# Optimization experiments

Hardware: AMD Instinct MI355X
Metric: run time of the kernel (lower is better)

## Reference

```python
import jax, jax.numpy as jnp
import numpy as np

Nc, Nt, K = 32, 64, 2
P = 1.0
BATCH = 4096
EPS_BIS = 1e-5
MAX_ITER = 100


def setup_inputs() -> dict:
    key = jax.random.key(0)
    ks = jax.random.split(key, 5)
    H = jax.random.normal(ks[0], (BATCH, K, Nc, 2 * Nt), dtype=jnp.float32)
    dims = [2 * K * K, 256, 256, 256, 4 * K]
    inp = {"H": H}
    for i in range(4):
        inp[f"W{i}"] = jax.random.normal(ks[1 + i], (dims[i], dims[i + 1]), dtype=jnp.float32) / float(np.sqrt(dims[i]))
        inp[f"b{i}"] = jnp.zeros((dims[i + 1],), dtype=jnp.float32)
    return inp


def _forward(H, W0, b0, W1, b1, W2, b2, W3, b3):
    batch = H.shape[0]
    eyeK = jnp.eye(K, dtype=jnp.complex64)
    # Source quirk: imag slice H[..., :Nt:2*Nt] has step 2*Nt>Nt -> only column 0, broadcast as imag part
    H1 = H[..., :Nt] + 1j * H[..., 0:Nt:2 * Nt]  # [b,K,Nc,Nt] complex64
    # Analog precoder: conj of center-subcarrier channel per user, unit-modulus normalized
    F_RF = jnp.conj(jnp.transpose(H1[:, :, Nc // 2, :], (0, 2, 1)))  # [b,Nt,K]
    F_RF = F_RF / jnp.abs(F_RF) / np.sqrt(Nt)
    # Source quirk: literal reshape (not permute) mixing batch and subcarrier dims
    H1r = H1.reshape(Nc, batch, K, Nt)
    H_equ = jnp.matmul(H1r, F_RF).reshape(batch, Nc, K, K)  # [Nc,b,K,Nt]@[b,Nt,K] -> [Nc,b,K,K]
    power = jnp.sum(jnp.abs(H_equ) ** 2, axis=(2, 3))  # [b,Nc]
    H_equ = H_equ / jnp.sqrt(power)[:, :, None, None]
    Hf = H_equ.reshape(batch, Nc, K * K)
    x = jnp.concatenate([jnp.real(Hf), jnp.imag(Hf)], axis=2)  # [b,Nc,2*K*K]
    # TRANS_BLOCK stand-in: MLP 8->256->256->256->4K
    for (Wl, bl, act) in ((W0, b0, True), (W1, b1, True), (W2, b2, True), (W3, b3, False)):
        x = x @ Wl + bl
        if act:
            x = jax.nn.relu(x)
    U = (x[..., 0:K] + 1j * x[..., K:2 * K]).astype(jnp.complex64)   # [b,Nc,K]
    Wm = (x[..., 2 * K:3 * K] + 1j * x[..., 3 * K:4 * K]).astype(jnp.complex64)
    Hc = H_equ.astype(jnp.complex64)  # H_hat
    coef = Wm * (jnp.abs(U) ** 2)     # [b,Nc,K]
    # B(mu) = sum_k W_k|U_k|^2 conj(h_k) h_k^T + K*mu*I  (mu*I added K times in source loop)
    B_base = jnp.einsum('bnk,bnki,bnkj->bnij', coef, jnp.conj(Hc), Hc)  # [b,Nc,K,K]
    UW = U * Wm

    def compute_V(mu, Bb, uw, hc):
        Bm = Bb + (K * mu) * eyeK
        Binv = jnp.linalg.inv(Bm)  # batched 2x2 complex inverse
        # V[:,:,i,k] = U_k W_k * (B^{-1} conj(h_k))_i
        return uw[:, :, None, :] * jnp.einsum('bnij,bnkj->bnik', Binv, jnp.conj(hc))

    # Bisection on mu for power constraint sum|V|^2 <= P
    def cond(s):
        lo, hi, mu, it = s
        return jnp.logical_and(hi - lo >= EPS_BIS, it <= MAX_ITER)

    def body(s):
        lo, hi, _, it = s
        mu = (lo + hi) / 2.0
        V = compute_V(mu, B_base, UW, Hc)
        Pitem = jnp.sum(jnp.abs(V) ** 2)
        big = Pitem > P
        return (jnp.where(big, mu, lo), jnp.where(big, hi, mu), mu, it + 1)

    init = (jnp.float32(0.0), jnp.float32(10.0), jnp.float32(5.0), jnp.int32(0))
    _, _, mu, _ = jax.lax.while_loop(cond, body, init)

    V = compute_V(mu, B_base, UW, Hc)  # [b,Nc,K,K]
    F_BB = V.reshape(Nc, batch, K, K)  # literal reshape, as in source
    F_SDMA = jnp.matmul(F_RF, F_BB).reshape(batch, Nc, Nt, K)
    Power = jnp.sum(jnp.abs(F_SDMA) ** 2, axis=(2, 3)).reshape(batch, Nc, 1, 1)
    F_BB = jnp.transpose(F_BB, (1, 0, 2, 3))
    F_BB = F_BB / jnp.sqrt(Power) * np.sqrt(K)
    F_BB = jnp.transpose(F_BB, (1, 0, 2, 3))
    F_SDMA = jnp.matmul(F_RF, F_BB)  # [Nc,b,Nt,K]
    F_SDMA = jnp.transpose(F_SDMA, (1, 0, 2, 3)).reshape(batch, K * Nc * Nt)
    return jnp.concatenate([jnp.real(F_SDMA), jnp.imag(F_SDMA)], axis=1)


def reference(H, W0, b0, W1, b1, W2, b2, W3, b3):
    return _forward(H, W0, b0, W1, b1, W2, b2, W3, b3)
```

## Files before the change

kernel.cpp:

```cpp
#include <hip/hip_runtime.h>

typedef _Float16 f16;
typedef __attribute__((ext_vector_type(8))) _Float16 f16x8;
typedef __attribute__((ext_vector_type(4))) _Float16 f16x4;
typedef __attribute__((ext_vector_type(4))) float f32x4;
typedef unsigned int u32;

#define M2N 131072
#define MFMA16 __builtin_amdgcn_mfma_f32_16x16x32_f16

struct C2 { float x, y; };
__device__ __forceinline__ C2 cmul(C2 a, C2 b){ C2 r; r.x = a.x*b.x - a.y*b.y; r.y = a.x*b.y + a.y*b.x; return r; }
__device__ __forceinline__ C2 cadd(C2 a, C2 b){ C2 r; r.x = a.x+b.x; r.y = a.y+b.y; return r; }
__device__ __forceinline__ C2 csub(C2 a, C2 b){ C2 r; r.x = a.x-b.x; r.y = a.y-b.y; return r; }
__device__ __forceinline__ C2 conjc(C2 a){ C2 r; r.x = a.x; r.y = -a.y; return r; }
__device__ __forceinline__ C2 cneg(C2 a){ C2 r; r.x = -a.x; r.y = -a.y; return r; }
__device__ __forceinline__ float cabs2(C2 a){ return a.x*a.x + a.y*a.y; }
__device__ __forceinline__ float dotr(C2 a, C2 b){ return a.x*b.x + a.y*b.y; }

__device__ __forceinline__ float wred(float v){
  #pragma unroll
  for (int s = 32; s > 0; s >>= 1) v += __shfl_xor(v, s, 64);
  return v;
}

__global__ void k_prep(const float* __restrict__ W0, const float* __restrict__ W1,
                       const float* __restrict__ W2, const float* __restrict__ W3,
                       f16* __restrict__ wfr12, f16* __restrict__ wfr0,
                       f16* __restrict__ wfr3, float* __restrict__ slots)
{
  const int b = blockIdx.x, tid = threadIdx.x;
  if (b < 64){
    const int slot = b*256 + tid;
    const int lane = slot & 63;
    const int rest = slot >> 6;
    const int kt = rest & 7, nt = (rest >> 3) & 15, L = rest >> 7;
    const float* W = L ? W2 : W1;
    const int n = nt*16 + (lane & 15);
    f16* dst = wfr12 + (size_t)rest*1024 + lane*8;
    #pragma unroll
    for (int e = 0; e < 8; ++e){
      const int k = kt*32 + (lane>>4)*8 + e;
      const float w = W[k*256 + n];
      const f16 h = (f16)w;
      dst[e] = h; dst[512+e] = (f16)(w - (float)h);
    }
  } else if (b == 64){
    for (int i = 0; i < 4; ++i){
      const int slot = i*256 + tid;
      const int lane = slot & 63, nt = slot >> 6;
      const int col = nt*16 + (lane & 15);
      f16* dst = wfr0 + (size_t)nt*1024 + lane*8;
      #pragma unroll
      for (int e = 0; e < 8; ++e){
        const int k = (lane>>4)*8 + e;
        const float w = (k < 8) ? W0[k*256 + col] : 0.f;
        const f16 h = (f16)w;
        dst[e] = h; dst[512+e] = (f16)(w - (float)h);
      }
    }
  } else {
    slots[tid] = 0.f;
    for (int i = 0; i < 2; ++i){
      const int slot = i*256 + tid;
      const int lane = slot & 63, kt = slot >> 6;
      const int col = lane & 15;
      f16* dst = wfr3 + (size_t)kt*1024 + lane*8;
      #pragma unroll
      for (int e = 0; e < 8; ++e){
        const int k = kt*32 + (lane>>4)*8 + e;
        const float w = (col < 8) ? W3[k*8 + col] : 0.f;
        const f16 h = (f16)w;
        dst[e] = h; dst[512+e] = (f16)(w - (float)h);
      }
    }
  }
}

__global__ void k_frf(const float* __restrict__ H, float2* __restrict__ frf,
                      float2* __restrict__ g2)
{
  const int b2 = blockIdx.x*2 + (threadIdx.x >> 7);
  const int tt = threadIdx.x & 127;
  const int t = tt >> 1, k = tt & 1;
  __shared__ float2 s[2][128];
  const size_t base = ((size_t)(b2*2 + k)*32 + 16)*128;
  const float are = H[base + t];
  const float aim = H[base];
  const float inv = rsqrtf(are*are + aim*aim) * 0.125f;
  float2 v; v.x = are*inv; v.y = -aim*inv;
  frf[((size_t)b2*64 + t)*2 + k] = v;
  s[threadIdx.x >> 7][tt] = v;
  __syncthreads();
  const int w = threadIdx.x >> 6;
  if ((w & 1) == 0){
    const int half = w >> 1;
    const int lane = threadIdx.x & 63;
    const float2 a = s[half][lane*2];
    const float2 b = s[half][lane*2 + 1];
    float re = a.x*b.x + a.y*b.y;
    float im = a.y*b.x - a.x*b.y;
    re = wred(re); im = wred(im);
    if (lane == 0){ float2 g; g.x = re; g.y = im; g2[blockIdx.x*2 + half] = g; }
  }
}

__global__ void k_hequ(const float* __restrict__ H, const float2* __restrict__ frf,
                       float* __restrict__ x)
{
  const int m2 = blockIdx.x*4 + (threadIdx.x >> 6);
  const int lane = threadIdx.x & 63;
  const int n = m2 >> 12, b2 = m2 & 4095;
  const float4 f = *(const float4*)(frf + ((size_t)b2*64 + lane)*2);
  float accr[2][2], acci[2][2];
  #pragma unroll
  for (int i = 0; i < 2; ++i){
    const float* hr = H + (size_t)(n*8192 + b2*2 + i) * 128;
    const float re = hr[lane];
    const float im = hr[0];
    accr[i][0] = re*f.x - im*f.y;  acci[i][0] = re*f.y + im*f.x;
    accr[i][1] = re*f.z - im*f.w;  acci[i][1] = re*f.w + im*f.z;
  }
  #pragma unroll
  for (int i = 0; i < 2; ++i)
    #pragma unroll
    for (int j = 0; j < 2; ++j){ accr[i][j] = wred(accr[i][j]); acci[i][j] = wred(acci[i][j]); }
  if (lane == 0){
    float pw = 0.f;
    #pragma unroll
    for (int i = 0; i < 2; ++i)
      #pragma unroll
      for (int j = 0; j < 2; ++j) pw += accr[i][j]*accr[i][j] + acci[i][j]*acci[i][j];
    const float rs = rsqrtf(pw);
    *(float4*)(x + (size_t)m2*8)     = make_float4(accr[0][0]*rs, accr[0][1]*rs, accr[1][0]*rs, accr[1][1]*rs);
    *(float4*)(x + (size_t)m2*8 + 4) = make_float4(acci[0][0]*rs, acci[0][1]*rs, acci[1][0]*rs, acci[1][1]*rs);
  }
}

#define SWX(r, c) ((r)*256 + ((c) ^ (((r)&7)<<3)))

__launch_bounds__(256, 3)
__global__ void k_mlp(const float* __restrict__ x, const f16* __restrict__ wfr12,
                      const f16* __restrict__ wfr0, const f16* __restrict__ wfr3,
                      const float* __restrict__ bias0, const float* __restrict__ bias1,
                      const float* __restrict__ bias2, const float* __restrict__ bias3,
                      float* __restrict__ y)
{
  __shared__ __align__(16) f16 xah[48*256];
  __shared__ __align__(16) f16 xal[48*256];
  const int tid = threadIdx.x, blk = blockIdx.x;
  const int lane = tid & 63, wv = tid >> 6;
  const int l15 = lane & 15, lh = lane >> 4;
  const int colb = wv*64;

  f32x4 acc[3][4];
  f16x8 ah[3], al[3], bh[4], bl[4];

  auto EPI = [&](){
    #pragma unroll
    for (int Mt = 0; Mt < 3; ++Mt)
      #pragma unroll
      for (int nt = 0; nt < 4; ++nt){
        f16x4 h4, l4;
        #pragma unroll
        for (int r = 0; r < 4; ++r){
          const float v = fmaxf(acc[Mt][nt][r], 0.f);
          const f16 h = (f16)v;
          h4[r] = h; l4[r] = (f16)(v - (float)h);
        }
        const int idx = SWX(Mt*16 + l15, colb + nt*16 + lh*4);
        *(f16x4*)(xah + idx) = h4;
        *(f16x4*)(xal + idx) = l4;
      }
  };

  #pragma unroll
  for (int nt = 0; nt < 4; ++nt){
    const f32x4 b4 = *(const f32x4*)(bias0 + colb + nt*16 + lh*4);
    #pragma unroll
    for (int Mt = 0; Mt < 3; ++Mt) acc[Mt][nt] = b4;
  }
  #pragma unroll
  for (int Mt = 0; Mt < 3; ++Mt){
    const int row = blk*48 + Mt*16 + l15;
    const float* xr = x + (size_t)row*8;
    const float4 v0 = *(const float4*)xr;
    const float4 v1 = *(const float4*)(xr+4);
    const float vv[8] = {v0.x,v0.y,v0.z,v0.w,v1.x,v1.y,v1.z,v1.w};
    #pragma unroll
    for (int e = 0; e < 8; ++e){
      const f16 h = (f16)vv[e];
      ah[Mt][e] = h; al[Mt][e] = (f16)(vv[e] - (float)h);
    }
  }
  #pragma unroll
  for (int nt = 0; nt < 4; ++nt){
    bh[nt] = *(const f16x8*)(wfr0 + (size_t)(wv*4+nt)*1024 + lane*8);
    bl[nt] = *(const f16x8*)(wfr0 + (size_t)(wv*4+nt)*1024 + 512 + lane*8);
  }
  #pragma unroll
  for (int Mt = 0; Mt < 3; ++Mt)
    #pragma unroll
    for (int nt = 0; nt < 4; ++nt){
      acc[Mt][nt] = MFMA16(bh[nt], ah[Mt], acc[Mt][nt], 0, 0, 0);
      acc[Mt][nt] = MFMA16(bh[nt], al[Mt], acc[Mt][nt], 0, 0, 0);
      acc[Mt][nt] = MFMA16(bl[nt], ah[Mt], acc[Mt][nt], 0, 0, 0);
    }
  EPI();
  __syncthreads();

  for (int L = 0; L < 2; ++L){
    const float* bs = L ? bias2 : bias1;
    #pragma unroll
    for (int nt = 0; nt < 4; ++nt){
      const f32x4 b4 = *(const f32x4*)(bs + colb + nt*16 + lh*4);
      #pragma unroll
      for (int Mt = 0; Mt < 3; ++Mt) acc[Mt][nt] = b4;
    }
    #pragma unroll 2
    for (int kt = 0; kt < 8; ++kt){
      #pragma unroll
      for (int Mt = 0; Mt < 3; ++Mt){
        const int idx = SWX(Mt*16 + l15, kt*32 + lh*8);
        ah[Mt] = *(const f16x8*)(xah + idx);
        al[Mt] = *(const f16x8*)(xal + idx);
      }
      #pragma unroll
      for (int nt = 0; nt < 4; ++nt){
        const size_t f = ((size_t)(L*128 + (wv*4+nt)*8 + kt))*1024;
        bh[nt] = *(const f16x8*)(wfr12 + f + lane*8);
        bl[nt] = *(const f16x8*)(wfr12 + f + 512 + lane*8);
      }
      #pragma unroll
      for (int Mt = 0; Mt < 3; ++Mt)
        #pragma unroll
        for (int nt = 0; nt < 4; ++nt){
          acc[Mt][nt] = MFMA16(bh[nt], ah[Mt], acc[Mt][nt], 0, 0, 0);
          acc[Mt][nt] = MFMA16(bh[nt], al[Mt], acc[Mt][nt], 0, 0, 0);
          acc[Mt][nt] = MFMA16(bl[nt], ah[Mt], acc[Mt][nt], 0, 0, 0);
        }
    }
    __syncthreads();
    EPI();
    __syncthreads();
  }

  f32x4 a3[3];
  {
    f32x4 b4 = {0.f, 0.f, 0.f, 0.f};
    if (lh < 2) b4 = *(const f32x4*)(bias3 + lh*4);
    #pragma unroll
    for (int Mt = 0; Mt < 3; ++Mt) a3[Mt] = b4;
  }
  #pragma unroll 2
  for (int kt = 0; kt < 8; ++kt){
    #pragma unroll
    for (int Mt = 0; Mt < 3; ++Mt){
      const int idx = SWX(Mt*16 + l15, kt*32 + lh*8);
      ah[Mt] = *(const f16x8*)(xah + idx);
      al[Mt] = *(const f16x8*)(xal + idx);
    }
    const f16x8 b3h = *(const f16x8*)(wfr3 + (size_t)kt*1024 + lane*8);
    const f16x8 b3l = *(const f16x8*)(wfr3 + (size_t)kt*1024 + 512 + lane*8);
    #pragma unroll
    for (int Mt = 0; Mt < 3; ++Mt){
      a3[Mt] = MFMA16(b3h, ah[Mt], a3[Mt], 0, 0, 0);
      a3[Mt] = MFMA16(b3h, al[Mt], a3[Mt], 0, 0, 0);
      a3[Mt] = MFMA16(b3l, ah[Mt], a3[Mt], 0, 0, 0);
    }
  }
  if (lh < 2){
    #pragma unroll
    for (int Mt = 0; Mt < 3; ++Mt){
      const int row = blk*48 + Mt*16 + l15;
      if (row < M2N) *(f32x4*)(y + (size_t)row*8 + lh*4) = a3[Mt];
    }
  }
}

struct Elem {
  C2 p[2][2], g[2][2], UW[2], d0, d1;
  float A0, A1, A2, c0, c1, c2, c3;
};
struct Coef { float A0, A1, A2, c0, c1, c2, c3; };

__device__ __forceinline__ void elem_core(const float* __restrict__ x,
                                          const float* __restrict__ y,
                                          int gid, Elem& E)
{
  const float4 xr = *(const float4*)(x + (size_t)gid*8);
  const float4 xi = *(const float4*)(x + (size_t)gid*8 + 4);
  C2 h[2][2];
  h[0][0].x = xr.x; h[0][0].y = xi.x; h[0][1].x = xr.y; h[0][1].y = xi.y;
  h[1][0].x = xr.z; h[1][0].y = xi.z; h[1][1].x = xr.w; h[1][1].y = xi.w;
  const float4 ya = *(const float4*)(y + (size_t)gid*8);
  const float4 yb = *(const float4*)(y + (size_t)gid*8 + 4);
  C2 U[2], Wm[2];
  U[0].x = ya.x; U[0].y = ya.z;  U[1].x = ya.y; U[1].y = ya.w;
  Wm[0].x = yb.x; Wm[0].y = yb.z; Wm[1].x = yb.y; Wm[1].y = yb.w;
  const float u20 = cabs2(U[0]), u21 = cabs2(U[1]);
  C2 cf[2];
  cf[0].x = Wm[0].x*u20; cf[0].y = Wm[0].y*u20;
  cf[1].x = Wm[1].x*u21; cf[1].y = Wm[1].y*u21;
  C2 B[2][2];
  #pragma unroll
  for (int i = 0; i < 2; ++i)
    #pragma unroll
    for (int j = 0; j < 2; ++j){
      const C2 t0 = cmul(conjc(h[0][i]), h[0][j]);
      const C2 t1 = cmul(conjc(h[1][i]), h[1][j]);
      B[i][j] = cadd(cmul(cf[0], t0), cmul(cf[1], t1));
    }
  C2 adj[2][2];
  adj[0][0] = B[1][1]; adj[0][1] = cneg(B[0][1]);
  adj[1][0] = cneg(B[1][0]); adj[1][1] = B[0][0];
  E.d0 = csub(cmul(B[0][0], B[1][1]), cmul(B[0][1], B[1][0]));
  E.d1.x = 2.f*(B[0][0].x + B[1][1].x);
  E.d1.y = 2.f*(B[0][0].y + B[1][1].y);
  #pragma unroll
  for (int k = 0; k < 2; ++k){
    #pragma unroll
    for (int j = 0; j < 2; ++j) E.g[k][j] = conjc(h[k][j]);
    #pragma unroll
    for (int i = 0; i < 2; ++i)
      E.p[k][i] = cadd(cmul(adj[i][0], E.g[k][0]), cmul(adj[i][1], E.g[k][1]));
    E.UW[k] = cmul(U[k], Wm[k]);
  }
  const float w0 = cabs2(E.UW[0]), w1 = cabs2(E.UW[1]);
  E.A0 = w0*(cabs2(E.p[0][0]) + cabs2(E.p[0][1])) + w1*(cabs2(E.p[1][0]) + cabs2(E.p[1][1]));
  E.A1 = 4.f*( w0*(dotr(E.p[0][0], E.g[0][0]) + dotr(E.p[0][1], E.g[0][1]))
             + w1*(dotr(E.p[1][0], E.g[1][0]) + dotr(E.p[1][1], E.g[1][1])) );
  E.A2 = 4.f*( w0*(cabs2(E.g[0][0]) + cabs2(E.g[0][1]))
             + w1*(cabs2(E.g[1][0]) + cabs2(E.g[1][1])) );
  E.c0 = cabs2(E.d0);
  E.c1 = 2.f*(E.d0.x*E.d1.x + E.d0.y*E.d1.y);
  E.c2 = cabs2(E.d1) + 8.f*E.d0.x;
  E.c3 = 8.f*E.d1.x;
}

__device__ __forceinline__ float evalf(float mu, const Coef& C){
  const float num = C.A0 + mu*(C.A1 + mu*C.A2);
  const float den = C.c0 + mu*(C.c1 + mu*(C.c2 + mu*(C.c3 + mu*16.f)));
  return num/den;
}

__device__ __forceinline__ void replay(const float* __restrict__ slots, int nrounds,
                                       float& lo, float& hi)
{
  const int DP[4] = {5, 5, 5, 4};
  for (int r = 0; r < nrounds; ++r){
    const float lo0 = lo, span = hi - lo;
    int k = 0;
    for (int d = 0; d < DP[r]; ++d){
      const float sd = span * (1.0f / (float)(1 << (d+1)));
      const float mu = fmaf((float)(2*k + 1), sd, lo0);
      const bool big = slots[r*32 + (1 << d) - 1 + k] > 1.0f;
      lo = big ? mu : lo;
      hi = big ? hi : mu;
      k = 2*k + (big ? 1 : 0);
    }
  }
}

__global__ void k_coef(const float* __restrict__ x, const float* __restrict__ y,
                       float* __restrict__ coef)
{
  const int gid = blockIdx.x*256 + threadIdx.x;
  Elem E;
  elem_core(x, y, gid, E);
  *(float4*)(coef + (size_t)gid*8)     = make_float4(E.A0, E.A1, E.A2, E.c0);
  *(float4*)(coef + (size_t)gid*8 + 4) = make_float4(E.c1, E.c2, E.c3, 0.f);
}

template<int ROUND, int D>
__global__ void k_red(const float* __restrict__ coef, float* __restrict__ slots)
{
  const int tid = threadIdx.x;
  const int gid = blockIdx.x*256 + tid;
  const int lane = tid & 63, wv = tid >> 6;
  __shared__ float r4[4][32];

  const float4 a = *(const float4*)(coef + (size_t)gid*8);
  const float4 b = *(const float4*)(coef + (size_t)gid*8 + 4);
  Coef C; C.A0 = a.x; C.A1 = a.y; C.A2 = a.z; C.c0 = a.w;
  C.c1 = b.x; C.c2 = b.y; C.c3 = b.z;

  float lo = 0.f, hi = 10.f;
  replay(slots, ROUND, lo, hi);

  const float lo0 = lo, span = hi - lo;
  int node = 0;
  #pragma unroll
  for (int d = 0; d < D; ++d){
    const float sd = span * (1.0f / (float)(1 << (d+1)));
    for (int k = 0; k < (1 << d); ++k){
      const float mu = fmaf((float)(2*k + 1), sd, lo0);
      const float f = wred(evalf(mu, C));
      if (lane == 0) r4[wv][node] = f;
      ++node;
    }
  }
  __syncthreads();
  if (tid < (1 << D) - 1)
    atomicAdd(&slots[ROUND*32 + tid], r4[0][tid] + r4[1][tid] + r4[2][tid] + r4[3][tid]);
}

__global__ void k_out(const float2* __restrict__ frf, const float* __restrict__ x,
                      const float* __restrict__ y, const float2* __restrict__ g2,
                      const float* __restrict__ slots, float* __restrict__ out)
{
  const int b2 = blockIdx.x;
  const int tid = threadIdx.x;
  __shared__ float Vs[32][8];
  __shared__ float scs[32];

  if (tid < 64){
    const int n = tid & 31;
    const bool isP = tid >= 32;
    const int gid = isP ? (b2*32 + n) : (n*4096 + b2);
    float lo = 0.f, hi = 10.f;
    replay(slots, 4, lo, hi);
    const float mu = 0.5f*(lo + hi);
    Elem E;
    elem_core(x, y, gid, E);
    C2 det; det.x = E.d0.x + mu*E.d1.x + 4.f*mu*mu; det.y = E.d0.y + mu*E.d1.y;
    const float id = 1.f/cabs2(det);
    C2 idet; idet.x = det.x*id; idet.y = -det.y*id;
    C2 Vv[2][2];
    #pragma unroll
    for (int k = 0; k < 2; ++k)
      #pragma unroll
      for (int i = 0; i < 2; ++i){
        C2 t; t.x = E.p[k][i].x + 2.f*mu*E.g[k][i].x; t.y = E.p[k][i].y + 2.f*mu*E.g[k][i].y;
        Vv[i][k] = cmul(E.UW[k], cmul(t, idet));
      }
    if (!isP){
      Vs[n][0] = Vv[0][0].x; Vs[n][1] = Vv[0][0].y;
      Vs[n][2] = Vv[0][1].x; Vs[n][3] = Vv[0][1].y;
      Vs[n][4] = Vv[1][0].x; Vs[n][5] = Vv[1][0].y;
      Vs[n][6] = Vv[1][1].x; Vs[n][7] = Vv[1][1].y;
    } else {
      const float2 gg2 = g2[gid & 4095];
      C2 gc; gc.x = gg2.x; gc.y = gg2.y;
      float P = 0.f;
      #pragma unroll
      for (int k = 0; k < 2; ++k){
        const C2 a = Vv[0][k], b = Vv[1][k];
        P += cabs2(a) + cabs2(b);
        const C2 t = cmul(gc, cmul(a, conjc(b)));
        P += 2.f*t.x;
      }
      scs[n] = 1.41421356237f * rsqrtf(P);
    }
  }
  __syncthreads();

  const int t = tid & 63;
  const int ng = tid >> 6;
  const float4 f = *(const float4*)(frf + ((size_t)b2*64 + t)*2);
  C2 f0, f1; f0.x = f.x; f0.y = f.y; f1.x = f.z; f1.y = f.w;
  for (int n = ng; n < 32; n += 4){
    C2 M00, M01, M10, M11;
    M00.x = Vs[n][0]; M00.y = Vs[n][1]; M01.x = Vs[n][2]; M01.y = Vs[n][3];
    M10.x = Vs[n][4]; M10.y = Vs[n][5]; M11.x = Vs[n][6]; M11.y = Vs[n][7];
    const float sc = scs[n];
    const C2 c0 = cadd(cmul(f0, M00), cmul(f1, M10));
    const C2 c1 = cadd(cmul(f0, M01), cmul(f1, M11));
    const size_t base = (size_t)b2*8192 + n*128 + t*2;
    *(float2*)(out + base)        = make_float2(c0.x*sc, c1.x*sc);
    *(float2*)(out + base + 4096) = make_float2(c0.y*sc, c1.y*sc);
  }
}

extern "C" void kernel_launch(void* const* d_in, const int* in_sizes, int n_in,
                              void* d_out, int out_size, void* d_ws, size_t ws_size,
                              hipStream_t stream)
{
  const float* H  = (const float*)d_in[0];
  const float* W0 = (const float*)d_in[1];
  const float* b0 = (const float*)d_in[2];
  const float* W1 = (const float*)d_in[3];
  const float* b1 = (const float*)d_in[4];
  const float* W2 = (const float*)d_in[5];
  const float* b2 = (const float*)d_in[6];
  const float* W3 = (const float*)d_in[7];
  const float* b3 = (const float*)d_in[8];
  float* out = (float*)d_out;
  char* ws = (char*)d_ws;
  (void)in_sizes; (void)n_in; (void)out_size; (void)ws_size;

  size_t o = 0;
  auto alloc = [&](size_t bytes) -> void* {
    void* p = ws + o;
    o += (bytes + 255) & ~(size_t)255;
    return p;
  };
  float2* frf   = (float2*)alloc((size_t)4096*64*2*sizeof(float2));
  float2* g2    = (float2*)alloc((size_t)4096*sizeof(float2));
  float*  xbuf  = (float*) alloc((size_t)M2N*8*sizeof(float));
  float*  ybuf  = (float*) alloc((size_t)M2N*8*sizeof(float));
  float*  coef  = (float*) alloc((size_t)M2N*8*sizeof(float));
  float*  slots = (float*) alloc(256*sizeof(float));
  f16*    wfr12 = (f16*)   alloc((size_t)256*1024*sizeof(f16));
  f16*    wfr0  = (f16*)   alloc((size_t)16*1024*sizeof(f16));
  f16*    wfr3  = (f16*)   alloc((size_t)8*1024*sizeof(f16));

  k_prep<<<66, 256, 0, stream>>>(W0, W1, W2, W3, wfr12, wfr0, wfr3, slots);
  k_frf<<<2048, 256, 0, stream>>>(H, frf, g2);
  k_hequ<<<32768, 256, 0, stream>>>(H, frf, xbuf);
  k_mlp<<<2731, 256, 0, stream>>>(xbuf, wfr12, wfr0, wfr3, b0, b1, b2, b3, ybuf);
  k_coef<<<512, 256, 0, stream>>>(xbuf, ybuf, coef);
  k_red<0,5><<<512, 256, 0, stream>>>(coef, slots);
  k_red<1,5><<<512, 256, 0, stream>>>(coef, slots);
  k_red<2,5><<<512, 256, 0, stream>>>(coef, slots);
  k_red<3,4><<<512, 256, 0, stream>>>(coef, slots);
  k_out<<<4096, 256, 0, stream>>>(frf, xbuf, ybuf, g2, slots, out);
}
```

Measured before the change: 277.3 us.

## Recompute analog precoder inline and fuse coef build into first bisection round

Removes the separate k_frf kernel and its frf buffer: the analog precoder is now recomputed from H inside k_hequ (which also emits g2 for n==0) and inside k_out (staged in shared memory). k_coef is merged into the first bisection-round kernel, so it builds coefficients and evaluates round 0 in one pass. Bisection slot replays now read from shared memory. This cuts two launches and one global round-trip, in exchange for redundant reads of H and recomputation of rsqrt in every k_hequ block.

```diff
diff --git a/kernel.cpp b/kernel.cpp
--- a/kernel.cpp
+++ b/kernel.cpp
@@ -22,6 +22,19 @@
   #pragma unroll
   for (int s = 32; s > 0; s >>= 1) v += __shfl_xor(v, s, 64);
   return v;
+}
+
+__device__ __forceinline__ float4 frf_inline(const float* __restrict__ H, int b2, int lane){
+  const size_t cb0 = ((size_t)(b2*2 + 0)*32 + 16)*128;
+  const size_t cb1 = ((size_t)(b2*2 + 1)*32 + 16)*128;
+  const float ar0 = H[cb0 + lane], ai0 = H[cb0];
+  const float ar1 = H[cb1 + lane], ai1 = H[cb1];
+  const float i0 = rsqrtf(ar0*ar0 + ai0*ai0) * 0.125f;
+  const float i1 = rsqrtf(ar1*ar1 + ai1*ai1) * 0.125f;
+  float4 f;
+  f.x = ar0*i0; f.y = -ai0*i0;
+  f.z = ar1*i1; f.w = -ai1*i1;
+  return f;
 }
 
 __global__ void k_prep(const float* __restrict__ W0, const float* __restrict__ W1,
@@ -77,41 +90,19 @@
   }
 }
 
-__global__ void k_frf(const float* __restrict__ H, float2* __restrict__ frf,
-                      float2* __restrict__ g2)
-{
-  const int b2 = blockIdx.x*2 + (threadIdx.x >> 7);
-  const int tt = threadIdx.x & 127;
-  const int t = tt >> 1, k = tt & 1;
-  __shared__ float2 s[2][128];
-  const size_t base = ((size_t)(b2*2 + k)*32 + 16)*128;
-  const float are = H[base + t];
-  const float aim = H[base];
-  const float inv = rsqrtf(are*are + aim*aim) * 0.125f;
-  float2 v; v.x = are*inv; v.y = -aim*inv;
-  frf[((size_t)b2*64 + t)*2 + k] = v;
-  s[threadIdx.x >> 7][tt] = v;
-  __syncthreads();
-  const int w = threadIdx.x >> 6;
-  if ((w & 1) == 0){
-    const int half = w >> 1;
-    const int lane = threadIdx.x & 63;
-    const float2 a = s[half][lane*2];
-    const float2 b = s[half][lane*2 + 1];
-    float re = a.x*b.x + a.y*b.y;
-    float im = a.y*b.x - a.x*b.y;
-    re = wred(re); im = wred(im);
-    if (lane == 0){ float2 g; g.x = re; g.y = im; g2[blockIdx.x*2 + half] = g; }
-  }
-}
-
-__global__ void k_hequ(const float* __restrict__ H, const float2* __restrict__ frf,
-                       float* __restrict__ x)
+__global__ void k_hequ(const float* __restrict__ H, float* __restrict__ x,
+                       float2* __restrict__ g2)
 {
   const int m2 = blockIdx.x*4 + (threadIdx.x >> 6);
   const int lane = threadIdx.x & 63;
   const int n = m2 >> 12, b2 = m2 & 4095;
-  const float4 f = *(const float4*)(frf + ((size_t)b2*64 + lane)*2);
+  const float4 f = frf_inline(H, b2, lane);
+  if (n == 0){
+    float re = f.x*f.z + f.y*f.w;
+    float im = f.y*f.z - f.x*f.w;
+    re = wred(re); im = wred(im);
+    if (lane == 0){ float2 g; g.x = re; g.y = im; g2[b2] = g; }
+  }
   float accr[2][2], acci[2][2];
   #pragma unroll
   for (int i = 0; i < 2; ++i){
@@ -362,32 +353,13 @@
   }
 }
 
-__global__ void k_coef(const float* __restrict__ x, const float* __restrict__ y,
-                       float* __restrict__ coef)
-{
-  const int gid = blockIdx.x*256 + threadIdx.x;
-  Elem E;
-  elem_core(x, y, gid, E);
-  *(float4*)(coef + (size_t)gid*8)     = make_float4(E.A0, E.A1, E.A2, E.c0);
-  *(float4*)(coef + (size_t)gid*8 + 4) = make_float4(E.c1, E.c2, E.c3, 0.f);
-}
-
-template<int ROUND, int D>
-__global__ void k_red(const float* __restrict__ coef, float* __restrict__ slots)
+template<int D>
+__device__ __forceinline__ void eval_round(const Coef& C, float lo, float hi,
+                                           float* __restrict__ slots, int roundBase,
+                                           float (*r4)[32])
 {
   const int tid = threadIdx.x;
-  const int gid = blockIdx.x*256 + tid;
   const int lane = tid & 63, wv = tid >> 6;
-  __shared__ float r4[4][32];
-
-  const float4 a = *(const float4*)(coef + (size_t)gid*8);
-  const float4 b = *(const float4*)(coef + (size_t)gid*8 + 4);
-  Coef C; C.A0 = a.x; C.A1 = a.y; C.A2 = a.z; C.c0 = a.w;
-  C.c1 = b.x; C.c2 = b.y; C.c3 = b.z;
-
-  float lo = 0.f, hi = 10.f;
-  replay(slots, ROUND, lo, hi);
-
   const float lo0 = lo, span = hi - lo;
   int node = 0;
   #pragma unroll
@@ -402,24 +374,66 @@
   }
   __syncthreads();
   if (tid < (1 << D) - 1)
-    atomicAdd(&slots[ROUND*32 + tid], r4[0][tid] + r4[1][tid] + r4[2][tid] + r4[3][tid]);
-}
-
-__global__ void k_out(const float2* __restrict__ frf, const float* __restrict__ x,
+    atomicAdd(&slots[roundBase + tid], r4[0][tid] + r4[1][tid] + r4[2][tid] + r4[3][tid]);
+}
+
+__launch_bounds__(256)
+__global__ void k_red0(const float* __restrict__ x, const float* __restrict__ y,
+                       float* __restrict__ coef, float* __restrict__ slots)
+{
+  const int gid = blockIdx.x*256 + threadIdx.x;
+  __shared__ float r4[4][32];
+  Elem E;
+  elem_core(x, y, gid, E);
+  *(float4*)(coef + (size_t)gid*8)     = make_float4(E.A0, E.A1, E.A2, E.c0);
+  *(float4*)(coef + (size_t)gid*8 + 4) = make_float4(E.c1, E.c2, E.c3, 0.f);
+  Coef C; C.A0 = E.A0; C.A1 = E.A1; C.A2 = E.A2; C.c0 = E.c0;
+  C.c1 = E.c1; C.c2 = E.c2; C.c3 = E.c3;
+  eval_round<5>(C, 0.f, 10.f, slots, 0, r4);
+}
+
+template<int ROUND, int D>
+__launch_bounds__(256)
+__global__ void k_red(const float* __restrict__ coef, float* __restrict__ slots)
+{
+  const int tid = threadIdx.x;
+  const int gid = blockIdx.x*256 + tid;
+  __shared__ float r4[4][32];
+  __shared__ float sl[96];
+  if (tid < ROUND*32) sl[tid] = slots[tid];
+
+  const float4 a = *(const float4*)(coef + (size_t)gid*8);
+  const float4 b = *(const float4*)(coef + (size_t)gid*8 + 4);
+  Coef C; C.A0 = a.x; C.A1 = a.y; C.A2 = a.z; C.c0 = a.w;
+  C.c1 = b.x; C.c2 = b.y; C.c3 = b.z;
+  __syncthreads();
+
+  float lo = 0.f, hi = 10.f;
+  replay(sl, ROUND, lo, hi);
+  eval_round<D>(C, lo, hi, slots, ROUND*32, r4);
+}
+
+__global__ void k_out(const float* __restrict__ H, const float* __restrict__ x,
                       const float* __restrict__ y, const float2* __restrict__ g2,
                       const float* __restrict__ slots, float* __restrict__ out)
 {
   const int b2 = blockIdx.x;
   const int tid = threadIdx.x;
+  __shared__ float4 fs[64];
   __shared__ float Vs[32][8];
   __shared__ float scs[32];
+  __shared__ float sl[128];
+
+  if (tid >= 128) sl[tid - 128] = slots[tid - 128];
+  if (tid < 64) fs[tid] = frf_inline(H, b2, tid);
+  __syncthreads();
 
   if (tid < 64){
     const int n = tid & 31;
     const bool isP = tid >= 32;
     const int gid = isP ? (b2*32 + n) : (n*4096 + b2);
     float lo = 0.f, hi = 10.f;
-    replay(slots, 4, lo, hi);
+    replay(sl, 4, lo, hi);
     const float mu = 0.5f*(lo + hi);
     Elem E;
     elem_core(x, y, gid, E);
@@ -457,7 +471,7 @@
 
   const int t = tid & 63;
   const int ng = tid >> 6;
-  const float4 f = *(const float4*)(frf + ((size_t)b2*64 + t)*2);
+  const float4 f = fs[t];
   C2 f0, f1; f0.x = f.x; f0.y = f.y; f1.x = f.z; f1.y = f.w;
   for (int n = ng; n < 32; n += 4){
     C2 M00, M01, M10, M11;
@@ -495,7 +509,6 @@
     o += (bytes + 255) & ~(size_t)255;
     return p;
   };
-  float2* frf   = (float2*)alloc((size_t)4096*64*2*sizeof(float2));
   float2* g2    = (float2*)alloc((size_t)4096*sizeof(float2));
   float*  xbuf  = (float*) alloc((size_t)M2N*8*sizeof(float));
   float*  ybuf  = (float*) alloc((size_t)M2N*8*sizeof(float));
@@ -506,13 +519,11 @@
   f16*    wfr3  = (f16*)   alloc((size_t)8*1024*sizeof(f16));
 
   k_prep<<<66, 256, 0, stream>>>(W0, W1, W2, W3, wfr12, wfr0, wfr3, slots);
-  k_frf<<<2048, 256, 0, stream>>>(H, frf, g2);
-  k_hequ<<<32768, 256, 0, stream>>>(H, frf, xbuf);
+  k_hequ<<<32768, 256, 0, stream>>>(H, xbuf, g2);
   k_mlp<<<2731, 256, 0, stream>>>(xbuf, wfr12, wfr0, wfr3, b0, b1, b2, b3, ybuf);
-  k_coef<<<512, 256, 0, stream>>>(xbuf, ybuf, coef);
-  k_red<0,5><<<512, 256, 0, stream>>>(coef, slots);
+  k_red0<<<512, 256, 0, stream>>>(xbuf, ybuf, coef, slots);
   k_red<1,5><<<512, 256, 0, stream>>>(coef, slots);
   k_red<2,5><<<512, 256, 0, stream>>>(coef, slots);
   k_red<3,4><<<512, 256, 0, stream>>>(coef, slots);
-  k_out<<<4096, 256, 0, stream>>>(frf, xbuf, ybuf, g2, slots, out);
-}
+  k_out<<<4096, 256, 0, stream>>>(H, xbuf, ybuf, g2, slots, out);
+}
```

After: 268.2 us. 3.3% less time.
